# Performance work log

Hardware: AMD Instinct MI355X
Metric: run time of the kernel (lower is better)

## Reference

```python
import jax, jax.numpy as jnp
import numpy as np

CONF_THRES = 0.596
IOU_THRES = 0.45
CELL_LIMIT = 200   # CELL_SIZE_LIMIT
MAX_CAND = 512     # fixed candidate pool for jit-able NMS
MAX_WH = 4096.0    # per-class NMS box offset (yolov5 trick)
NEG_SLOPE = 0.01   # LeakyReLU default


def xywh2xyxy(b):
    cx, cy, w, h = b[..., 0], b[..., 1], b[..., 2], b[..., 3]
    return jnp.stack([cx - w / 2, cy - h / 2, cx + w / 2, cy + h / 2], axis=-1)


def box_iou(a, b):
    # a:[N,4] b:[M,4] xyxy -> [N,M]
    area_a = (a[:, 2] - a[:, 0]) * (a[:, 3] - a[:, 1])
    area_b = (b[:, 2] - b[:, 0]) * (b[:, 3] - b[:, 1])
    lt = jnp.maximum(a[:, None, :2], b[None, :, :2])
    rb = jnp.minimum(a[:, None, 2:], b[None, :, 2:])
    wh = jnp.clip(rb - lt, 0.0)
    inter = wh[..., 0] * wh[..., 1]
    return inter / (area_a[:, None] + area_b[None, :] - inter + 1e-9)


def nms_single(pred):
    # pred [N,85]: xywh, obj, 80 class probs (yolov5 layout)
    obj = pred[:, 4]
    conf_cls = pred[:, 5:] * obj[:, None]
    conf = conf_cls.max(-1)
    cls = jnp.argmax(conf_cls, -1).astype(jnp.float32)
    box = xywh2xyxy(pred[:, :4])
    score = jnp.where(conf > CONF_THRES, conf, -1.0)
    order = jnp.argsort(-score)[:MAX_CAND]          # top candidates, score-sorted
    boxes, scores, cls = box[order], score[order], cls[order]
    off = boxes + cls[:, None] * MAX_WH             # per-class offset
    iou = box_iou(off, off)
    idx = jnp.arange(MAX_CAND)
    def body(i, keep):
        sup = (iou[i] > IOU_THRES) & (idx > i) & keep[i]
        return keep & ~sup
    keep = jax.lax.fori_loop(0, MAX_CAND, body, scores > 0.0)  # greedy NMS
    ks = jnp.where(keep, scores, -1.0)
    top = jnp.argsort(-ks)[:CELL_LIMIT]
    return boxes[top], ks[top] > 0.0                # [200,4], [200]


def roi_align_1x1(feat, boxes, scale):
    # feat [C,H,W]; boxes [M,4] xyxy image pixels; output_size=1, 2x2 bilinear samples
    C, H, W = feat.shape
    b = boxes * scale
    x1, y1 = b[:, 0], b[:, 1]
    bw = jnp.maximum(b[:, 2] - x1, 1.0)
    bh = jnp.maximum(b[:, 3] - y1, 1.0)
    g = jnp.array([0.25, 0.75], dtype=feat.dtype)   # (i+0.5)/2 sample offsets
    xs = x1[:, None] + g[None, :] * bw[:, None]     # [M,2]
    ys = y1[:, None] + g[None, :] * bh[:, None]
    X = jnp.tile(xs, (1, 2))                        # [M,4] x varies fast
    Y = jnp.repeat(ys, 2, axis=1)
    X = jnp.clip(X, 0.0, W - 1.0)
    Y = jnp.clip(Y, 0.0, H - 1.0)
    x0 = jnp.floor(X).astype(jnp.int32); y0 = jnp.floor(Y).astype(jnp.int32)
    x1i = jnp.minimum(x0 + 1, W - 1); y1i = jnp.minimum(y0 + 1, H - 1)
    wx = X - x0; wy = Y - y0
    v = (feat[:, y0, x0] * ((1 - wy) * (1 - wx))[None]
         + feat[:, y0, x1i] * ((1 - wy) * wx)[None]
         + feat[:, y1i, x0] * (wy * (1 - wx))[None]
         + feat[:, y1i, x1i] * (wy * wx)[None])     # [C,M,4]
    return v.mean(-1).T                             # [M,C]


def reference(out, x1, x2, x3, x4, W1, b1, W2, b2):
    Himg = x1.shape[-2] * 8
    Wimg = x1.shape[-1] * 8
    whwh = jnp.array([Wimg, Himg, Wimg, Himg], dtype=jnp.float32)
    boxes, mask = jax.vmap(nms_single)(out)         # [B,200,4], [B,200]

    def per_img(f1, f2, f3, f4, bb):
        r = jnp.concatenate([
            roi_align_1x1(f1, bb, 1 / 8),
            roi_align_1x1(f2, bb, 1 / 16),
            roi_align_1x1(f3, bb, 1 / 32),
            roi_align_1x1(f4, bb, 1 / 64)], axis=-1)          # [200,1920]
        h = jax.nn.leaky_relu(r @ W1 + b1, NEG_SLOPE)
        h = jax.nn.leaky_relu(h @ W2 + b2, NEG_SLOPE)
        return jnp.concatenate([bb / whwh, h], axis=-1)        # [200,68]

    feats = jax.vmap(per_img)(x1, x2, x3, x4, boxes)
    feats = feats * mask[..., None].astype(feats.dtype)       # zero padded rows
    return feats, mask


def setup_inputs() -> dict:
    key = jax.random.key(0)
    ks = jax.random.split(key, 10)
    B, IMG = 8, 1024
    N = ((IMG // 8) ** 2 + (IMG // 16) ** 2 + (IMG // 32) ** 2) * 3  # 64512
    cxcy = jax.random.uniform(ks[0], (B, N, 2)) * IMG
    wh = jax.random.uniform(ks[1], (B, N, 2)) * 240.0 + 16.0
    obj = jax.random.uniform(ks[2], (B, N, 1))
    cls = jax.random.uniform(ks[3], (B, N, 80))
    out = jnp.concatenate([cxcy, wh, obj, cls], axis=-1)
    x1 = jax.random.normal(ks[4], (B, 128, 128, 128), dtype=jnp.float32)
    x2 = jax.random.normal(ks[5], (B, 256, 64, 64), dtype=jnp.float32)
    x3 = jax.random.normal(ks[6], (B, 512, 32, 32), dtype=jnp.float32)
    x4 = jax.random.normal(ks[7], (B, 1024, 16, 16), dtype=jnp.float32)
    W1 = jax.random.normal(ks[8], (1920, 64)) * 0.02
    b1 = jnp.zeros((64,), jnp.float32)
    W2 = jax.random.normal(ks[9], (64, 64)) * 0.1
    b2 = jnp.zeros((64,), jnp.float32)
    return dict(out=out, x1=x1, x2=x2, x3=x3, x4=x4, W1=W1, b1=b1, W2=W2, b2=b2)
```

## Files before the change

### kernel.cpp

```cpp
#include <hip/hip_runtime.h>
#include <hip/hip_bf16.h>

typedef unsigned int u32;
typedef unsigned long long u64;

#define B_IMG 8
#define N_ANCH 64512
#define NCLS 80
#define ROW 85
#define CONF_T 0.596f
#define IOU_T 0.45f
#define MAXC 512
#define CELL 200
#define CAP 4096

__device__ __forceinline__ float fsub(float a, float b){ return __fsub_rn(a,b); }
__device__ __forceinline__ float fadd(float a, float b){ return __fadd_rn(a,b); }
__device__ __forceinline__ float fmul(float a, float b){ return __fmul_rn(a,b); }

__device__ __forceinline__ u64 shfl_u64(u64 v, int src) {
    u32 lo = (u32)(v & 0xFFFFFFFFull), hi = (u32)(v >> 32);
    lo = (u32)__shfl((int)lo, src);
    hi = (u32)__shfl((int)hi, src);
    return ((u64)hi << 32) | (u64)lo;
}

__global__ __launch_bounds__(256) void k_score(const float* __restrict__ outp,
                                               float* __restrict__ scores,
                                               u32* __restrict__ hist) {
    int tid = threadIdx.x;
    int gi = blockIdx.x * 64 + (tid >> 2);
    int q = tid & 3;
    const float* row = outp + (size_t)gi * ROW;

    float v1  = row[q + 4];
    float v2  = row[q + 8];
    float v3  = row[q + 12];
    float v4  = row[q + 16];
    float v5  = row[q + 20];
    float v6  = row[q + 24];
    float v7  = row[q + 28];
    float v8  = row[q + 32];
    float v9  = row[q + 36];
    float v10 = row[q + 40];
    float v11 = row[q + 44];
    float v12 = row[q + 48];
    float v13 = row[q + 52];
    float v14 = row[q + 56];
    float v15 = row[q + 60];
    float v16 = row[q + 64];
    float v17 = row[q + 68];
    float v18 = row[q + 72];
    float v19 = row[q + 76];
    float v20 = row[q + 80];
    float v84 = row[84];

    float m = (q == 0) ? -1e30f : v1;
#define MXS(x) { m = ((x) > m) ? (x) : m; }
    MXS(v2)  MXS(v3)  MXS(v4)  MXS(v5)  MXS(v6)  MXS(v7)  MXS(v8)
    MXS(v9)  MXS(v10) MXS(v11) MXS(v12) MXS(v13) MXS(v14) MXS(v15)
    MXS(v16) MXS(v17) MXS(v18) MXS(v19) MXS(v20) MXS(v84)
#undef MXS

    float o1 = __shfl_xor(m, 1); m = (o1 > m) ? o1 : m;
    float o2 = __shfl_xor(m, 2); m = (o2 > m) ? o2 : m;

    int lane = tid & 63;
    float obj = __shfl(v1, lane & ~3);

    float conf = fmul(m, obj);
    float score = (conf > CONF_T) ? conf : -1.0f;

    if (q == 0) {
        scores[gi] = score;
        if (score > 0.0f) {
            int b = gi / N_ANCH;
            atomicAdd(&hist[(size_t)b * 65536 + (__float_as_uint(score) >> 16)], 1u);
        }
    }
}

__global__ __launch_bounds__(256) void k_thresh(const u32* __restrict__ hist,
                                                u32* __restrict__ thresh) {
    int b = blockIdx.x;
    int tid = threadIdx.x;
    __shared__ u32 csum[256];
    const u32* h = hist + (size_t)b * 65536;
    u32 s = 0;
    for (int i = 0; i < 256; ++i) s += h[tid * 256 + i];
    csum[tid] = s;
    __syncthreads();
    if (tid == 0) {
        u32 cum = 0;
        int ch = 255;
        for (; ch >= 0; --ch) {
            if (cum + csum[ch] >= MAXC) break;
            cum += csum[ch];
        }
        if (ch < 0) { thresh[b] = 0u; return; }
        u32 c2 = cum;
        int bkt = ch * 256 + 255;
        for (; bkt >= ch * 256; --bkt) {
            c2 += h[bkt];
            if (c2 >= MAXC) break;
        }
        thresh[b] = ((u32)bkt) << 16;
    }
}

__global__ __launch_bounds__(256) void k_compact(const float* __restrict__ scores,
                                                 const u32* __restrict__ thresh,
                                                 u32* __restrict__ cnt,
                                                 u64* __restrict__ list) {
    int i = blockIdx.x * blockDim.x + threadIdx.x;
    if (i >= B_IMG * N_ANCH) return;
    float s = scores[i];
    if (s <= 0.0f) return;
    int b = i / N_ANCH;
    u32 key = __float_as_uint(s);
    if (key < thresh[b]) return;
    u32 pos = atomicAdd(&cnt[b], 1u);
    if (pos < CAP) {
        u32 n = (u32)(i - b * N_ANCH);
        list[(size_t)b * CAP + pos] = ((u64)key << 32) | (u64)(0xFFFFFFFFu - n);
    }
}

__global__ __launch_bounds__(512) void k_sort(const float* __restrict__ outp,
                                              const u32* __restrict__ cnt,
                                              const u64* __restrict__ list,
                                              float* __restrict__ oboxw,
                                              float* __restrict__ areaw,
                                              float* __restrict__ bxw,
                                              u32* __restrict__ nvalidw) {
    __shared__ u64 buf[CAP];
    int b = blockIdx.x;
    int tid = threadIdx.x;

    int M = (int)min(cnt[b], (u32)CAP);
    int P = MAXC;
    while (P < M) P <<= 1;

    for (int t = tid; t < P; t += 512)
        buf[t] = (t < M) ? list[(size_t)b * CAP + t] : 0ull;
    __syncthreads();

    for (int k = 2; k <= P; k <<= 1) {
        for (int j = k >> 1; j > 0; j >>= 1) {
            for (int t = tid; t < P; t += 512) {
                int ixj = t ^ j;
                if (ixj > t) {
                    u64 a = buf[t], c = buf[ixj];
                    bool desc = ((t & k) == 0);
                    if (desc ? (a < c) : (a > c)) { buf[t] = c; buf[ixj] = a; }
                }
            }
            __syncthreads();
        }
    }

    int nvalid = min(M, MAXC);
    bool valid = (tid < nvalid);
    u32 n = 0;
    if (valid) n = 0xFFFFFFFFu - (u32)(buf[tid] & 0xFFFFFFFFull);

    float bx0, bx1, bx2, bx3;
    float ob0, ob1, ob2, ob3;
    if (valid) {
        const float* p = outp + ((size_t)b * N_ANCH + n) * ROW;
        float cx = p[0], cy = p[1], w = p[2], h = p[3], obj = p[4];
        float best = -1.0f; int bi = 0;
        for (int c = 0; c < NCLS; ++c) {
            float v = fmul(p[5 + c], obj);
            if (v > best) { best = v; bi = c; }
        }
        float hw = fmul(w, 0.5f), hh = fmul(h, 0.5f);
        bx0 = fsub(cx, hw); bx1 = fsub(cy, hh);
        bx2 = fadd(cx, hw); bx3 = fadd(cy, hh);
        float off = fmul((float)bi, 4096.0f);
        ob0 = fadd(bx0, off); ob1 = fadd(bx1, off);
        ob2 = fadd(bx2, off); ob3 = fadd(bx3, off);
    } else {
        bx0 = bx1 = bx2 = bx3 = 0.0f;
        ob0 = ob1 = ob2 = ob3 = -1.0e6f;
    }
    ((float4*)oboxw)[b * MAXC + tid] = make_float4(ob0, ob1, ob2, ob3);
    areaw[b * MAXC + tid] = fmul(fsub(ob2, ob0), fsub(ob3, ob1));
    ((float4*)bxw)[b * MAXC + tid] = make_float4(bx0, bx1, bx2, bx3);
    if (tid == 0) nvalidw[b] = (u32)nvalid;
}

__global__ __launch_bounds__(64) void k_iou(const float* __restrict__ oboxw,
                                            const float* __restrict__ areaw,
                                            u64* __restrict__ sup) {
    int t = blockIdx.x, b = blockIdx.y;
    int ti = 0;
    while (t >= 8 - ti) { t -= 8 - ti; ++ti; }
    int tj = ti + t;

    int lane = threadIdx.x;
    int i = ti * 64 + lane;
    float4 oi = ((const float4*)oboxw)[b * MAXC + i];
    float ai = areaw[b * MAXC + i];

    __shared__ float jb[5][64];
    int jg = tj * 64 + lane;
    float4 oj = ((const float4*)oboxw)[b * MAXC + jg];
    jb[0][lane] = oj.x; jb[1][lane] = oj.y;
    jb[2][lane] = oj.z; jb[3][lane] = oj.w;
    jb[4][lane] = areaw[b * MAXC + jg];
    __syncthreads();

    u64 bits = 0;
    for (int jl = 0; jl < 64; ++jl) {
        int j = tj * 64 + jl;
        float ltx = fmaxf(oi.x, jb[0][jl]);
        float lty = fmaxf(oi.y, jb[1][jl]);
        float rbx = fminf(oi.z, jb[2][jl]);
        float rby = fminf(oi.w, jb[3][jl]);
        float ww = fmaxf(fsub(rbx, ltx), 0.0f);
        float hh2 = fmaxf(fsub(rby, lty), 0.0f);
        float inter = fmul(ww, hh2);
        float denom = fadd(fsub(fadd(ai, jb[4][jl]), inter), 1e-9f);
        float iou = __fdiv_rn(inter, denom);
        if ((j > i) && (iou > IOU_T)) bits |= (1ull << jl);
    }

    u64* sr = sup + ((size_t)(b * MAXC + i)) * 8;
    if (ti == tj) {
        for (int w = 0; w < ti; ++w) sr[w] = 0ull;
    }
    sr[tj] = bits;
}

#define GW(W, KW, NE, APPLY) \
    { u64 todo = (KW) & (NE); \
      while (todo) { \
          int bb = (int)__builtin_ctzll(todo); \
          const u64* rr = srow + (((W) * 64 + bb) * 8); \
          u64 hm = (bb < 63) ? (~0ull << (bb + 1)) : 0ull; \
          KW &= ~(rr[W] & hm); \
          APPLY \
          todo &= hm & KW; \
      } }

__global__ __launch_bounds__(512) void k_greedy(const u64* __restrict__ sup,
                                                const u32* __restrict__ nvalidw,
                                                const float* __restrict__ bxw,
                                                float* __restrict__ selbox,
                                                u32* __restrict__ selcnt,
                                                float* __restrict__ mask_out) {
    __shared__ u64 srow[MAXC * 8];
    __shared__ u64 neword[8];
    __shared__ u64 keepw[8];
    int b = blockIdx.x;
    int tid = threadIdx.x;
    int nvalid = (int)nvalidw[b];

    const u64* g = sup + (size_t)b * MAXC * 8;
    u64 r0 = g[tid*8+0], r1 = g[tid*8+1], r2 = g[tid*8+2], r3 = g[tid*8+3];
    u64 r4 = g[tid*8+4], r5 = g[tid*8+5], r6 = g[tid*8+6], r7 = g[tid*8+7];
    srow[tid*8+0]=r0; srow[tid*8+1]=r1; srow[tid*8+2]=r2; srow[tid*8+3]=r3;
    srow[tid*8+4]=r4; srow[tid*8+5]=r5; srow[tid*8+6]=r6; srow[tid*8+7]=r7;
    bool ne = ((r0|r1|r2|r3|r4|r5|r6|r7) != 0ull);
    u64 bal = __ballot(ne);
    if ((tid & 63) == 0) neword[tid >> 6] = bal;
    if (tid < 8) {
        int lo = tid * 64;
        u64 kw = 0;
        if (nvalid >= lo + 64) kw = ~0ull;
        else if (nvalid > lo) kw = (1ull << (nvalid - lo)) - 1ull;
        keepw[tid] = kw;
    }
    __syncthreads();

    if (tid == 0) {
        u64 k0=keepw[0], k1=keepw[1], k2=keepw[2], k3=keepw[3];
        u64 k4=keepw[4], k5=keepw[5], k6=keepw[6], k7=keepw[7];
        u64 n0=neword[0], n1=neword[1], n2=neword[2], n3=neword[3];
        u64 n4=neword[4], n5=neword[5], n6=neword[6], n7=neword[7];
        GW(0, k0, n0, k1&=~rr[1]; k2&=~rr[2]; k3&=~rr[3]; k4&=~rr[4]; k5&=~rr[5]; k6&=~rr[6]; k7&=~rr[7];)
        GW(1, k1, n1, k2&=~rr[2]; k3&=~rr[3]; k4&=~rr[4]; k5&=~rr[5]; k6&=~rr[6]; k7&=~rr[7];)
        GW(2, k2, n2, k3&=~rr[3]; k4&=~rr[4]; k5&=~rr[5]; k6&=~rr[6]; k7&=~rr[7];)
        GW(3, k3, n3, k4&=~rr[4]; k5&=~rr[5]; k6&=~rr[6]; k7&=~rr[7];)
        GW(4, k4, n4, k5&=~rr[5]; k6&=~rr[6]; k7&=~rr[7];)
        GW(5, k5, n5, k6&=~rr[6]; k7&=~rr[7];)
        GW(6, k6, n6, k7&=~rr[7];)
        GW(7, k7, n7, )
        keepw[0]=k0; keepw[1]=k1; keepw[2]=k2; keepw[3]=k3;
        keepw[4]=k4; keepw[5]=k5; keepw[6]=k6; keepw[7]=k7;
    }
    __syncthreads();

    int w = tid >> 6, l = tid & 63;
    bool kept = (tid < nvalid) && ((keepw[w] >> l) & 1ull);
    int rank = 0;
    for (int ww = 0; ww < w; ++ww) rank += __popcll(keepw[ww]);
    rank += __popcll(keepw[w] & ((l == 0) ? 0ull : ((1ull << l) - 1ull)));
    if (kept && rank < CELL) {
        float4 bx = ((const float4*)bxw)[b * MAXC + tid];
        float* sb = selbox + ((size_t)b * CELL + rank) * 4;
        sb[0] = bx.x; sb[1] = bx.y; sb[2] = bx.z; sb[3] = bx.w;
        mask_out[b * CELL + rank] = 1.0f;
    }
    if (tid == 0) {
        int tot = 0;
        for (int ww = 0; ww < 8; ++ww) tot += __popcll(keepw[ww]);
        selcnt[b] = (u32)min(tot, CELL);
    }
}

__global__ __launch_bounds__(512) void k_nms(const float* __restrict__ outp,
                                             const u32* __restrict__ cnt,
                                             const u64* __restrict__ list,
                                             float* __restrict__ selbox,
                                             u32* __restrict__ selcnt,
                                             float* __restrict__ mask_out) {
    __shared__ u64 buf[CAP];
    __shared__ float obox[MAXC][4];
    __shared__ float area[MAXC];
    __shared__ u64 keepw[8];
    int b = blockIdx.x;
    int tid = threadIdx.x;

    int M = (int)min(cnt[b], (u32)CAP);
    int P = MAXC;
    while (P < M) P <<= 1;

    for (int t = tid; t < P; t += 512)
        buf[t] = (t < M) ? list[(size_t)b * CAP + t] : 0ull;
    __syncthreads();

    for (int k = 2; k <= P; k <<= 1) {
        for (int j = k >> 1; j > 0; j >>= 1) {
            for (int t = tid; t < P; t += 512) {
                int ixj = t ^ j;
                if (ixj > t) {
                    u64 a = buf[t], c = buf[ixj];
                    bool desc = ((t & k) == 0);
                    if (desc ? (a < c) : (a > c)) { buf[t] = c; buf[ixj] = a; }
                }
            }
            __syncthreads();
        }
    }

    int nvalid = min(M, MAXC);
    bool valid = (tid < nvalid);
    u32 n = 0;
    if (valid) n = 0xFFFFFFFFu - (u32)(buf[tid] & 0xFFFFFFFFull);
    __syncthreads();

    float bx0, bx1, bx2, bx3;
    float ob0, ob1, ob2, ob3;
    if (valid) {
        const float* p = outp + ((size_t)b * N_ANCH + n) * ROW;
        float cx = p[0], cy = p[1], w = p[2], h = p[3], obj = p[4];
        float best = -1.0f; int bi = 0;
        for (int c = 0; c < NCLS; ++c) {
            float v = fmul(p[5 + c], obj);
            if (v > best) { best = v; bi = c; }
        }
        float hw = fmul(w, 0.5f), hh = fmul(h, 0.5f);
        bx0 = fsub(cx, hw); bx1 = fsub(cy, hh);
        bx2 = fadd(cx, hw); bx3 = fadd(cy, hh);
        float off = fmul((float)bi, 4096.0f);
        ob0 = fadd(bx0, off); ob1 = fadd(bx1, off);
        ob2 = fadd(bx2, off); ob3 = fadd(bx3, off);
    } else {
        bx0 = bx1 = bx2 = bx3 = 0.0f;
        ob0 = ob1 = ob2 = ob3 = -1.0e6f;
    }
    obox[tid][0] = ob0; obox[tid][1] = ob1;
    obox[tid][2] = ob2; obox[tid][3] = ob3;
    area[tid] = fmul(fsub(ob2, ob0), fsub(ob3, ob1));
    __syncthreads();

    u64* sup = buf;
    {
        u64 rowb[8] = {0,0,0,0,0,0,0,0};
        float aa = area[tid];
        for (int j = tid + 1; j < MAXC; ++j) {
            float ltx = fmaxf(ob0, obox[j][0]);
            float lty = fmaxf(ob1, obox[j][1]);
            float rbx = fminf(ob2, obox[j][2]);
            float rby = fminf(ob3, obox[j][3]);
            float ww = fmaxf(fsub(rbx, ltx), 0.0f);
            float hh2 = fmaxf(fsub(rby, lty), 0.0f);
            float inter = fmul(ww, hh2);
            float denom = fadd(fsub(fadd(aa, area[j]), inter), 1e-9f);
            float iou = __fdiv_rn(inter, denom);
            if (iou > IOU_T) rowb[j >> 6] |= (1ull << (j & 63));
        }
        for (int w2 = 0; w2 < 8; ++w2) sup[tid * 8 + w2] = rowb[w2];
    }
    __syncthreads();

    if (tid < 64) {
        int lane = tid;
        u64 kw = 0;
        if (lane < 8) {
            int lo = lane * 64;
            if (nvalid >= lo + 64) kw = ~0ull;
            else if (nvalid > lo) kw = (1ull << (nvalid - lo)) - 1ull;
        }
        for (int i = 0; i < MAXC; ++i) {
            u64 wv = shfl_u64(kw, i >> 6);
            if ((wv >> (i & 63)) & 1ull) {
                if (lane < 8) kw &= ~sup[(size_t)i * 8 + lane];
            }
        }
        if (lane < 8) keepw[lane] = kw;
    }
    __syncthreads();

    int w = tid >> 6, l = tid & 63;
    bool kept = valid && ((keepw[w] >> l) & 1ull);
    int rank = 0;
    for (int ww = 0; ww < w; ++ww) rank += __popcll(keepw[ww]);
    rank += __popcll(keepw[w] & ((l == 0) ? 0ull : ((1ull << l) - 1ull)));
    if (kept && rank < CELL) {
        float* sb = selbox + ((size_t)b * CELL + rank) * 4;
        sb[0] = bx0; sb[1] = bx1; sb[2] = bx2; sb[3] = bx3;
        mask_out[b * CELL + rank] = 1.0f;
    }
    if (tid == 0) {
        int tot = 0;
        for (int ww = 0; ww < 8; ++ww) tot += __popcll(keepw[ww]);
        selcnt[b] = (u32)min(tot, CELL);
    }
}

__global__ __launch_bounds__(256) void k_roi_gather(
        const float* __restrict__ x1, const float* __restrict__ x2,
        const float* __restrict__ x3, const float* __restrict__ x4,
        const float* __restrict__ selbox, const u32* __restrict__ selcnt,
        float* __restrict__ rws) {
    int slot = blockIdx.y;
    int b = blockIdx.z;
    if (slot >= (int)selcnt[b]) return;

    int unit = blockIdx.x * 256 + threadIdx.x;
    int c = unit >> 2;
    int p = unit & 3;

    const float* fb; int Wd; float s; int cl;
    if (c < 128)      { fb = x1 + (size_t)b * 128 * 128 * 128; Wd = 128; s = 0.125f;    cl = c; }
    else if (c < 384) { fb = x2 + (size_t)b * 256 * 64 * 64;   Wd = 64;  s = 0.0625f;   cl = c - 128; }
    else if (c < 896) { fb = x3 + (size_t)b * 512 * 32 * 32;   Wd = 32;  s = 0.03125f;  cl = c - 384; }
    else              { fb = x4 + (size_t)b * 1024 * 16 * 16;  Wd = 16;  s = 0.015625f; cl = c - 896; }

    const float* sb = selbox + ((size_t)b * CELL + slot) * 4;
    float box0 = sb[0], box1 = sb[1], box2 = sb[2], box3 = sb[3];

    float bx1f = box0 * s, by1f = box1 * s;
    float bw = fmaxf(box2 * s - bx1f, 1.0f);
    float bh = fmaxf(box3 * s - by1f, 1.0f);
    float gx = (p & 1)  ? 0.75f : 0.25f;
    float gy = (p >> 1) ? 0.75f : 0.25f;
    float X = bx1f + gx * bw;
    float Y = by1f + gy * bh;
    X = fminf(fmaxf(X, 0.0f), (float)(Wd - 1));
    Y = fminf(fmaxf(Y, 0.0f), (float)(Wd - 1));
    int x0 = (int)floorf(X), y0 = (int)floorf(Y);
    int x1i = min(x0 + 1, Wd - 1), y1i = min(y0 + 1, Wd - 1);
    float wx = X - (float)x0, wy = Y - (float)y0;

    const float* f = fb + (size_t)cl * Wd * Wd;
    float v = f[y0 * Wd + x0]  * ((1.0f - wy) * (1.0f - wx))
            + f[y0 * Wd + x1i] * ((1.0f - wy) * wx)
            + f[y1i * Wd + x0] * (wy * (1.0f - wx))
            + f[y1i * Wd + x1i]* (wy * wx);

    int lane = threadIdx.x & 63;
    int base = lane & ~3;
    float v0 = __shfl(v, base + 0);
    float v1 = __shfl(v, base + 1);
    float v2 = __shfl(v, base + 2);
    float v3 = __shfl(v, base + 3);
    if (p == 0) {
        rws[((size_t)b * CELL + slot) * 1920 + c] = (((v0 + v1) + v2) + v3) * 0.25f;
    }
}

__global__ __launch_bounds__(256) void k_mlp(
        const float* __restrict__ W1, const float* __restrict__ b1,
        const float* __restrict__ W2, const float* __restrict__ b2,
        const float* __restrict__ selbox, const u32* __restrict__ selcnt,
        const float* __restrict__ rws, float* __restrict__ feats) {
    int slot = blockIdx.x;
    int b = blockIdx.y;
    if (slot >= (int)selcnt[b]) return;
    int tid = threadIdx.x;

    __shared__ float psum[4][64];
    __shared__ float h1[64];

    const float* r = rws + ((size_t)b * CELL + slot) * 1920;

    int j = tid & 63, part = tid >> 6;
    {
        float acc = 0.0f;
        int k0 = part * 480;
        for (int k = k0; k < k0 + 480; ++k)
            acc += r[k] * W1[(size_t)k * 64 + j];
        psum[part][j] = acc;
    }
    __syncthreads();
    if (tid < 64) {
        float v = psum[0][tid] + psum[1][tid] + psum[2][tid] + psum[3][tid] + b1[tid];
        h1[tid] = (v >= 0.0f) ? v : 0.01f * v;
    }
    __syncthreads();

    float* orow = feats + ((size_t)b * CELL + slot) * 68;
    if (tid < 64) {
        float acc = b2[tid];
        for (int k = 0; k < 64; ++k) acc += h1[k] * W2[k * 64 + tid];
        float v = (acc >= 0.0f) ? acc : 0.01f * acc;
        orow[4 + tid] = v;
    }
    if (tid < 4) {
        const float* sb = selbox + ((size_t)b * CELL + slot) * 4;
        orow[tid] = sb[tid] * (1.0f / 1024.0f);
    }
}

__global__ __launch_bounds__(256) void k_roi_mlp(
        const float* __restrict__ x1, const float* __restrict__ x2,
        const float* __restrict__ x3, const float* __restrict__ x4,
        const float* __restrict__ W1, const float* __restrict__ b1,
        const float* __restrict__ W2, const float* __restrict__ b2,
        const float* __restrict__ selbox, const u32* __restrict__ selcnt,
        float* __restrict__ feats) {
    int slot = blockIdx.x;
    int b = blockIdx.y;
    if (slot >= (int)selcnt[b]) return;
    int tid = threadIdx.x;

    __shared__ float r[1920];
    __shared__ float psum[4][64];
    __shared__ float h1[64];

    const float* sb = selbox + ((size_t)b * CELL + slot) * 4;
    float box0 = sb[0], box1 = sb[1], box2 = sb[2], box3 = sb[3];

    const float* feat[4] = {
        x1 + (size_t)b * 128 * 128 * 128,
        x2 + (size_t)b * 256 * 64 * 64,
        x3 + (size_t)b * 512 * 32 * 32,
        x4 + (size_t)b * 1024 * 16 * 16
    };
    const int   Cs[4]  = {128, 256, 512, 1024};
    const int   Wd_[4] = {128, 64, 32, 16};
    const float Ss[4]  = {0.125f, 0.0625f, 0.03125f, 0.015625f};
    const int   Off[4] = {0, 128, 384, 896};

    for (int lvl = 0; lvl < 4; ++lvl) {
        int Wd = Wd_[lvl], C = Cs[lvl];
        float s = Ss[lvl];
        float bx1f = box0 * s, by1f = box1 * s;
        float bw = fmaxf(box2 * s - bx1f, 1.0f);
        float bh = fmaxf(box3 * s - by1f, 1.0f);
        float xs[2] = { bx1f + 0.25f * bw, bx1f + 0.75f * bw };
        float ys[2] = { by1f + 0.25f * bh, by1f + 0.75f * bh };
        int idx[4][4]; float wt[4][4];
        for (int p = 0; p < 4; ++p) {
            float X = xs[p & 1], Y = ys[p >> 1];
            X = fminf(fmaxf(X, 0.0f), (float)(Wd - 1));
            Y = fminf(fmaxf(Y, 0.0f), (float)(Wd - 1));
            int x0 = (int)floorf(X), y0 = (int)floorf(Y);
            int x1i = min(x0 + 1, Wd - 1), y1i = min(y0 + 1, Wd - 1);
            float wx = X - (float)x0, wy = Y - (float)y0;
            idx[p][0] = y0 * Wd + x0;  idx[p][1] = y0 * Wd + x1i;
            idx[p][2] = y1i * Wd + x0; idx[p][3] = y1i * Wd + x1i;
            wt[p][0] = (1.0f - wy) * (1.0f - wx); wt[p][1] = (1.0f - wy) * wx;
            wt[p][2] = wy * (1.0f - wx);          wt[p][3] = wy * wx;
        }
        const float* fb = feat[lvl];
        int HW = Wd * Wd;
        for (int c = tid; c < C; c += 256) {
            const float* f = fb + (size_t)c * HW;
            float acc = 0.0f;
            for (int p = 0; p < 4; ++p)
                acc += f[idx[p][0]] * wt[p][0] + f[idx[p][1]] * wt[p][1]
                     + f[idx[p][2]] * wt[p][2] + f[idx[p][3]] * wt[p][3];
            r[Off[lvl] + c] = acc * 0.25f;
        }
    }
    __syncthreads();

    int j = tid & 63, part = tid >> 6;
    {
        float acc = 0.0f;
        int k0 = part * 480;
        for (int k = k0; k < k0 + 480; ++k)
            acc += r[k] * W1[(size_t)k * 64 + j];
        psum[part][j] = acc;
    }
    __syncthreads();
    if (tid < 64) {
        float v = psum[0][tid] + psum[1][tid] + psum[2][tid] + psum[3][tid] + b1[tid];
        h1[tid] = (v >= 0.0f) ? v : 0.01f * v;
    }
    __syncthreads();

    float* orow = feats + ((size_t)b * CELL + slot) * 68;
    if (tid < 64) {
        float acc = b2[tid];
        for (int k = 0; k < 64; ++k) acc += h1[k] * W2[k * 64 + tid];
        float v = (acc >= 0.0f) ? acc : 0.01f * acc;
        orow[4 + tid] = v;
    }
    if (tid < 4) {
        float bv = (tid == 0) ? box0 : (tid == 1) ? box1 : (tid == 2) ? box2 : box3;
        orow[tid] = bv * (1.0f / 1024.0f);
    }
}

extern "C" void kernel_launch(void* const* d_in, const int* in_sizes, int n_in,
                              void* d_out, int out_size, void* d_ws, size_t ws_size,
                              hipStream_t stream) {
    const float* outp = (const float*)d_in[0];
    const float* x1 = (const float*)d_in[1];
    const float* x2 = (const float*)d_in[2];
    const float* x3 = (const float*)d_in[3];
    const float* x4 = (const float*)d_in[4];
    const float* W1 = (const float*)d_in[5];
    const float* b1 = (const float*)d_in[6];
    const float* W2 = (const float*)d_in[7];
    const float* b2 = (const float*)d_in[8];

    char* ws = (char*)d_ws;
    const size_t o_hist   = 0;
    const size_t o_cnt    = 2097152;
    const size_t o_thresh = 2097152 + 256;
    const size_t o_scores = 2097152 + 512;
    const size_t o_list   = o_scores + 2064384;
    const size_t o_selbox = o_list + 262144;
    const size_t o_selcnt = o_selbox + 25600;
    const size_t o_rws    = o_selcnt + 256;
    const size_t ws_need_rws = o_rws + (size_t)B_IMG * CELL * 1920 * 4;
    const size_t o_sup    = ws_need_rws;
    const size_t o_obox   = o_sup + 262144;
    const size_t o_area   = o_obox + 65536;
    const size_t o_bx     = o_area + 16384;
    const size_t o_nvalid = o_bx + 65536;
    const size_t ws_need_full = o_nvalid + 256;

    u32*   hist   = (u32*)(ws + o_hist);
    u32*   cnt    = (u32*)(ws + o_cnt);
    u32*   thresh = (u32*)(ws + o_thresh);
    float* scores = (float*)(ws + o_scores);
    u64*   list   = (u64*)(ws + o_list);
    float* selbox = (float*)(ws + o_selbox);
    u32*   selcnt = (u32*)(ws + o_selcnt);
    float* rws    = (float*)(ws + o_rws);
    u64*   sup    = (u64*)(ws + o_sup);
    float* oboxw  = (float*)(ws + o_obox);
    float* areaw  = (float*)(ws + o_area);
    float* bxw    = (float*)(ws + o_bx);
    u32*   nvalidw= (u32*)(ws + o_nvalid);

    float* feats = (float*)d_out;
    float* mask  = feats + (size_t)B_IMG * CELL * 68;

    hipMemsetAsync(d_out, 0, (size_t)out_size * sizeof(float), stream);
    hipMemsetAsync(ws, 0, 2097152 + 512, stream);

    int total = B_IMG * N_ANCH;
    int blocks = (total + 255) / 256;
    int score_blocks = total / 64;
    k_score  <<<score_blocks, 256, 0, stream>>>(outp, scores, hist);
    k_thresh <<<B_IMG, 256, 0, stream>>>(hist, thresh);
    k_compact<<<blocks, 256, 0, stream>>>(scores, thresh, cnt, list);

    if (ws_size >= ws_need_full) {
        k_sort  <<<B_IMG, 512, 0, stream>>>(outp, cnt, list, oboxw, areaw, bxw, nvalidw);
        k_iou   <<<dim3(36, B_IMG), 64, 0, stream>>>(oboxw, areaw, sup);
        k_greedy<<<B_IMG, 512, 0, stream>>>(sup, nvalidw, bxw, selbox, selcnt, mask);
    } else {
        k_nms   <<<B_IMG, 512, 0, stream>>>(outp, cnt, list, selbox, selcnt, mask);
    }

    if (ws_size >= ws_need_rws) {
        k_roi_gather<<<dim3(30, CELL, B_IMG), 256, 0, stream>>>(
            x1, x2, x3, x4, selbox, selcnt, rws);
        k_mlp<<<dim3(CELL, B_IMG), 256, 0, stream>>>(
            W1, b1, W2, b2, selbox, selcnt, rws, feats);
    } else {
        k_roi_mlp<<<dim3(CELL, B_IMG), 256, 0, stream>>>(
            x1, x2, x3, x4, W1, b1, W2, b2, selbox, selcnt, feats);
    }
}
```

Before: 408.0 us.

## Skip class reads for low-objectness rows and shrink score histogram

The score kernel now reads objectness first and loads the 80 class probabilities only when objectness exceeds the confidence threshold, since conf = obj*max_cls can't pass otherwise. The 65536-bucket per-image histogram is replaced by 128 buckets starting at the bit pattern of the threshold, with overflow clamped into the top bucket. This shrinks the workspace memset and the threshold scan. The early-out is exact because class probabilities are at most 1. The clamped top bucket can make the threshold coarser if many scores fall into it, but compaction keeps all keys at or above the threshold, so this is still safe.

```diff
diff --git a/kernel.cpp b/kernel.cpp
--- a/kernel.cpp
+++ b/kernel.cpp
@@ -14,6 +14,9 @@
 #define CELL 200
 #define CAP 4096
 
+#define HBKT 128
+#define KEYBASE 0x3F18u
+
 __device__ __forceinline__ float fsub(float a, float b){ return __fsub_rn(a,b); }
 __device__ __forceinline__ float fadd(float a, float b){ return __fadd_rn(a,b); }
 __device__ __forceinline__ float fmul(float a, float b){ return __fmul_rn(a,b); }
@@ -33,78 +36,72 @@
     int q = tid & 3;
     const float* row = outp + (size_t)gi * ROW;
 
-    float v1  = row[q + 4];
-    float v2  = row[q + 8];
-    float v3  = row[q + 12];
-    float v4  = row[q + 16];
-    float v5  = row[q + 20];
-    float v6  = row[q + 24];
-    float v7  = row[q + 28];
-    float v8  = row[q + 32];
-    float v9  = row[q + 36];
-    float v10 = row[q + 40];
-    float v11 = row[q + 44];
-    float v12 = row[q + 48];
-    float v13 = row[q + 52];
-    float v14 = row[q + 56];
-    float v15 = row[q + 60];
-    float v16 = row[q + 64];
-    float v17 = row[q + 68];
-    float v18 = row[q + 72];
-    float v19 = row[q + 76];
-    float v20 = row[q + 80];
-    float v84 = row[84];
-
-    float m = (q == 0) ? -1e30f : v1;
+    float obj = row[4];
+    float score = -1.0f;
+
+    if (obj > CONF_T) {
+        float v1  = row[q + 4];
+        float v2  = row[q + 8];
+        float v3  = row[q + 12];
+        float v4  = row[q + 16];
+        float v5  = row[q + 20];
+        float v6  = row[q + 24];
+        float v7  = row[q + 28];
+        float v8  = row[q + 32];
+        float v9  = row[q + 36];
+        float v10 = row[q + 40];
+        float v11 = row[q + 44];
+        float v12 = row[q + 48];
+        float v13 = row[q + 52];
+        float v14 = row[q + 56];
+        float v15 = row[q + 60];
+        float v16 = row[q + 64];
+        float v17 = row[q + 68];
+        float v18 = row[q + 72];
+        float v19 = row[q + 76];
+        float v20 = row[q + 80];
+        float v84 = row[84];
+
+        float m = (q == 0) ? -1e30f : v1;
 #define MXS(x) { m = ((x) > m) ? (x) : m; }
-    MXS(v2)  MXS(v3)  MXS(v4)  MXS(v5)  MXS(v6)  MXS(v7)  MXS(v8)
-    MXS(v9)  MXS(v10) MXS(v11) MXS(v12) MXS(v13) MXS(v14) MXS(v15)
-    MXS(v16) MXS(v17) MXS(v18) MXS(v19) MXS(v20) MXS(v84)
+        MXS(v2)  MXS(v3)  MXS(v4)  MXS(v5)  MXS(v6)  MXS(v7)  MXS(v8)
+        MXS(v9)  MXS(v10) MXS(v11) MXS(v12) MXS(v13) MXS(v14) MXS(v15)
+        MXS(v16) MXS(v17) MXS(v18) MXS(v19) MXS(v20) MXS(v84)
 #undef MXS
 
-    float o1 = __shfl_xor(m, 1); m = (o1 > m) ? o1 : m;
-    float o2 = __shfl_xor(m, 2); m = (o2 > m) ? o2 : m;
-
-    int lane = tid & 63;
-    float obj = __shfl(v1, lane & ~3);
-
-    float conf = fmul(m, obj);
-    float score = (conf > CONF_T) ? conf : -1.0f;
+        float o1 = __shfl_xor(m, 1); m = (o1 > m) ? o1 : m;
+        float o2 = __shfl_xor(m, 2); m = (o2 > m) ? o2 : m;
+
+        float conf = fmul(m, obj);
+        score = (conf > CONF_T) ? conf : -1.0f;
+    }
 
     if (q == 0) {
         scores[gi] = score;
         if (score > 0.0f) {
             int b = gi / N_ANCH;
-            atomicAdd(&hist[(size_t)b * 65536 + (__float_as_uint(score) >> 16)], 1u);
-        }
-    }
-}
-
-__global__ __launch_bounds__(256) void k_thresh(const u32* __restrict__ hist,
+            u32 bk = (__float_as_uint(score) >> 16) - KEYBASE;
+            if (bk > HBKT - 1) bk = HBKT - 1;
+            atomicAdd(&hist[(size_t)b * HBKT + bk], 1u);
+        }
+    }
+}
+
+__global__ __launch_bounds__(128) void k_thresh(const u32* __restrict__ hist,
                                                 u32* __restrict__ thresh) {
     int b = blockIdx.x;
     int tid = threadIdx.x;
-    __shared__ u32 csum[256];
-    const u32* h = hist + (size_t)b * 65536;
-    u32 s = 0;
-    for (int i = 0; i < 256; ++i) s += h[tid * 256 + i];
-    csum[tid] = s;
+    __shared__ u32 h[HBKT];
+    h[tid] = hist[(size_t)b * HBKT + tid];
     __syncthreads();
     if (tid == 0) {
-        u32 cum = 0;
-        int ch = 255;
-        for (; ch >= 0; --ch) {
-            if (cum + csum[ch] >= MAXC) break;
-            cum += csum[ch];
-        }
-        if (ch < 0) { thresh[b] = 0u; return; }
-        u32 c2 = cum;
-        int bkt = ch * 256 + 255;
-        for (; bkt >= ch * 256; --bkt) {
+        u32 c2 = 0;
+        int bkt = HBKT - 1;
+        for (; bkt >= 0; --bkt) {
             c2 += h[bkt];
             if (c2 >= MAXC) break;
         }
-        thresh[b] = ((u32)bkt) << 16;
+        thresh[b] = (bkt < 0) ? 0u : (((u32)bkt + KEYBASE) << 16);
     }
 }
 
@@ -632,10 +629,10 @@
     const float* b2 = (const float*)d_in[8];
 
     char* ws = (char*)d_ws;
-    const size_t o_hist   = 0;
-    const size_t o_cnt    = 2097152;
-    const size_t o_thresh = 2097152 + 256;
-    const size_t o_scores = 2097152 + 512;
+    const size_t o_cnt    = 0;
+    const size_t o_hist   = 256;
+    const size_t o_thresh = 4352;
+    const size_t o_scores = 4608;
     const size_t o_list   = o_scores + 2064384;
     const size_t o_selbox = o_list + 262144;
     const size_t o_selcnt = o_selbox + 25600;
@@ -648,8 +645,8 @@
     const size_t o_nvalid = o_bx + 65536;
     const size_t ws_need_full = o_nvalid + 256;
 
+    u32*   cnt    = (u32*)(ws + o_cnt);
     u32*   hist   = (u32*)(ws + o_hist);
-    u32*   cnt    = (u32*)(ws + o_cnt);
     u32*   thresh = (u32*)(ws + o_thresh);
     float* scores = (float*)(ws + o_scores);
     u64*   list   = (u64*)(ws + o_list);
@@ -666,13 +663,13 @@
     float* mask  = feats + (size_t)B_IMG * CELL * 68;
 
     hipMemsetAsync(d_out, 0, (size_t)out_size * sizeof(float), stream);
-    hipMemsetAsync(ws, 0, 2097152 + 512, stream);
+    hipMemsetAsync(ws, 0, 4608, stream);
 
     int total = B_IMG * N_ANCH;
     int blocks = (total + 255) / 256;
     int score_blocks = total / 64;
     k_score  <<<score_blocks, 256, 0, stream>>>(outp, scores, hist);
-    k_thresh <<<B_IMG, 256, 0, stream>>>(hist, thresh);
+    k_thresh <<<B_IMG, 128, 0, stream>>>(hist, thresh);
     k_compact<<<blocks, 256, 0, stream>>>(scores, thresh, cnt, list);
 
     if (ws_size >= ws_need_full) {
```

Result: faster. 357.2 us (-12.5%).
